# Optimization experiments

Hardware: AMD Instinct MI355X
Metric: run time of the kernel (lower is better)

Reference implementation:

```python
import jax, jax.numpy as jnp
import numpy as np

NEG_SLOPE = 0.2
K_L = 0.5
K_G = 0.5
TEMP_G = 1e-3


def _leaky(v):
    return jnp.where(v >= 0, v, NEG_SLOPE * v)


def _topk_row_mask(scores, keep):
    # scores: [n, n, h]; torch.topk(dim=0) -> indices [keep, n] per head,
    # then head_mask[indices, :] = 1 selects whole ROWS (any column hit).
    n = scores.shape[0]
    s = jnp.transpose(scores, (1, 2, 0))        # [n_cols, h, n_rows]
    _, idx = jax.lax.top_k(s, keep)             # [n_cols, h, keep]

    def per_head(idx_h):                        # idx_h: [n_cols, keep]
        return jnp.zeros((n,), scores.dtype).at[idx_h.reshape(-1)].set(1.0)

    rows = jax.vmap(per_head, in_axes=1, out_axes=0)(idx)  # [h, n_rows]
    return jnp.transpose(rows)[:, None, :]      # [n_rows, 1, h] broadcast over cols


def setup_inputs() -> dict:
    key = jax.random.key(0)
    ks = jax.random.split(key, 8)
    n, in_f, feat_dim = 1024, 256, 128
    H, F = 4, 64                                # n_heads, n_hidden (out_features=256)
    feats = jax.random.normal(ks[0], (n, feat_dim), dtype=jnp.float32)
    x = jax.random.normal(ks[1], (n, in_f), dtype=jnp.float32)
    adj = jax.random.randint(ks[2], (n, n, 1), 0, 2).astype(jnp.int32)
    sc = 0.05
    W_l = jax.random.normal(ks[3], (in_f, H * F), dtype=jnp.float32) * sc
    W_r = jax.random.normal(ks[4], (in_f, H * F), dtype=jnp.float32) * sc
    attn_w = jax.random.normal(ks[5], (F,), dtype=jnp.float32) * sc
    W_delta = jax.random.normal(ks[6], (2 * F, F), dtype=jnp.float32) * sc
    b_delta = jnp.zeros((F,), dtype=jnp.float32)
    return {"feats": feats, "x": x, "adj": adj, "W_l": W_l, "W_r": W_r,
            "attn_w": attn_w, "W_delta": W_delta, "b_delta": b_delta}


def reference(feats, x, adj, W_l, W_r, attn_w, W_delta, b_delta):
    n = x.shape[0]
    F = attn_w.shape[0]
    H = W_l.shape[1] // F
    g_l = (x @ W_l).reshape(n, H, F)
    g_r = (x @ W_r).reshape(n, H, F)
    # g_sum[i, j] = g_l[j] + g_r[i]  (repeat vs repeat_interleave ordering)
    g_sum = g_r[:, None, :, :] + g_l[None, :, :, :]          # [n, n, H, F]
    e = jnp.einsum('ijhf,f->ijh', _leaky(g_sum), attn_w)     # [n, n, H]

    mask_adj = adj > 0                                        # [n, n, 1]
    a_l = jax.nn.softmax(jnp.where(mask_adj, e, -jnp.inf), axis=1)
    a_1nd = a_l * mask_adj.astype(e.dtype)

    keep_l = int(n * (1.0 - K_L))
    a_filt = a_1nd * _topk_row_mask(a_1nd, keep_l)
    attn_local = jnp.einsum('ijh,jhf->ihf', a_filt, g_r)     # [n, H, F]

    omega = jax.nn.softmax(e, axis=1)
    fn = (feats - feats.min(axis=0)) / (feats.max(axis=0) - feats.min(axis=0))
    fn = jnp.where(jnp.isnan(fn), 0.0, fn)
    g_rn = (g_r - g_r.min(axis=0)) / (g_r.max(axis=0) - g_r.min(axis=0))
    nf = jnp.linalg.norm(fn, axis=1)                          # [n] (index j)
    ng = jnp.linalg.norm(g_rn, axis=2)                        # [n, H] (index i)
    alpha = jax.nn.softmax(jnp.abs(nf[None, :, None] - ng[:, None, :]), axis=1)
    gamma = 0.5 * (omega + (1.0 - alpha))

    keep_g = int(n * (1.0 - K_G))
    gf = gamma * _topk_row_mask(gamma, keep_g)
    gf = jax.nn.softmax(jnp.where(gf == 0, 1e-10, gf) / TEMP_G, axis=1)
    attn_global = jnp.einsum('ijh,jhf->ihf', gf, g_r)         # [n, H, F]

    inter = _leaky(jnp.concatenate([attn_local, attn_global], axis=2) @ W_delta + b_delta)
    delta = jax.nn.softmax(inter, axis=1)                     # softmax over heads (torch dim=1)
    attn_res = delta * attn_local + (1.0 - delta) * attn_global
    return attn_res.reshape(n, H * F)
```

## Files before the change

kernel.cpp:

```cpp
#include <hip/hip_runtime.h>
#include <cstdint>
#include <cstddef>

#define N 1024
#define HN 4
#define FDIM 64
#define KSEL 512
#define FLT_MAX_ 3.402823466e+38f

__device__ __forceinline__ float wred_sum(float v){
#pragma unroll
  for(int o=32;o>0;o>>=1) v += __shfl_down(v,o,64);
  return v;
}
__device__ __forceinline__ float bfly_sum(float v){
#pragma unroll
  for(int o=1;o<64;o<<=1) v += __shfl_xor(v,o,64);
  return v;
}
__device__ __forceinline__ float bfly_max(float v){
#pragma unroll
  for(int o=1;o<64;o<<=1) v = fmaxf(v,__shfl_xor(v,o,64));
  return v;
}
__device__ __forceinline__ int bfly_sumi(int v){
#pragma unroll
  for(int o=1;o<64;o<<=1) v += __shfl_xor(v,o,64);
  return v;
}
__device__ __forceinline__ float bred_sum(float v, float* scr){
  int t=threadIdx.x;
  v = wred_sum(v);
  __syncthreads();
  if((t&63)==0) scr[t>>6]=v;
  __syncthreads();
  return (scr[0]+scr[1])+(scr[2]+scr[3]);
}

__global__ __launch_bounds__(256) void stage1(const float* __restrict__ x,
                                              const float* __restrict__ W_l,
                                              const float* __restrict__ W_r,
                                              const int* __restrict__ adj,
                                              const float* __restrict__ feats,
                                              float* __restrict__ g_l,
                                              float* __restrict__ g_r,
                                              unsigned* __restrict__ adjbit,
                                              int* __restrict__ masks,
                                              float* __restrict__ pmin_f,
                                              float* __restrict__ pmax_f){
  int bx = blockIdx.x, t = threadIdx.x;
  if(bx < 512){
    const float* __restrict__ W = (bx >= 256) ? W_r : W_l;
    float* __restrict__ g = (bx >= 256) ? g_r : g_l;
    int i0 = (bx & 255)*4;
    float acc[4] = {0.f,0.f,0.f,0.f};
#pragma unroll 8
    for(int k=0;k<256;k++){
      float w = W[(size_t)k*256 + t];
#pragma unroll
      for(int r=0;r<4;r++) acc[r] = fmaf(x[(size_t)(i0+r)*256 + k], w, acc[r]);
    }
#pragma unroll
    for(int r=0;r<4;r++) g[(size_t)(i0+r)*256 + t] = acc[r];
  } else if(bx < 1536){
    int i = bx - 512, w = t>>6, lane = t&63;
    if(i < 32) masks[i*256 + t] = 0;
#pragma unroll
    for(int it=0; it<4; it++){
      int j = w*256 + it*64 + lane;
      int v = adj[(size_t)i*N + j];
      unsigned long long mb = __ballot(v > 0);
      if(lane == 0){
        adjbit[i*32 + w*8 + it*2]     = (unsigned)mb;
        adjbit[i*32 + w*8 + it*2 + 1] = (unsigned)(mb >> 32);
      }
    }
  } else {
    int chunk = bx - 1536;
    if(t < 128){
      float lo = FLT_MAX_, hi = -FLT_MAX_;
      int r0 = chunk*64;
      for(int r=0;r<64;r++){
        float v = feats[(size_t)(r0+r)*128 + t];
        lo = fminf(lo,v); hi = fmaxf(hi,v);
      }
      pmin_f[chunk*128+t]=lo; pmax_f[chunk*128+t]=hi;
    }
  }
}

__global__ __launch_bounds__(256) void stage2(const float* __restrict__ g_l,
                                              const float* __restrict__ g_r,
                                              const float* __restrict__ attn_w,
                                              const float* __restrict__ feats,
                                              const float* __restrict__ pmin_f, const float* __restrict__ pmax_f,
                                              float* __restrict__ pmin_g, float* __restrict__ pmax_g,
                                              float* __restrict__ nf,
                                              float* __restrict__ e){
  __shared__ __align__(16) float smem[2*64*68 + 128];
  int bx = blockIdx.x, t = threadIdx.x;
  if(bx < 1024){
    float* grs = smem;
    float* gls = smem + 64*68;
    float* aw  = smem + 2*64*68;
    float* aw2 = aw + 64;
    int h = bx >> 8, i0 = ((bx>>4)&15)*64, j0 = (bx&15)*64;
    if(t < 64){ float w = attn_w[t]; aw[t]=w; aw2[t]=0.2f*w; }
#pragma unroll
    for(int k=0;k<16;k++){
      int idx = t + k*256; int r = idx>>6, f = idx&63;
      grs[r*68+f] = g_r[(size_t)(i0+r)*256 + h*64 + f];
      gls[r*68+f] = g_l[(size_t)(j0+r)*256 + h*64 + f];
    }
    __syncthreads();
    int tj = t&15, ti = t>>4;
    float acc[4][4];
#pragma unroll
    for(int a=0;a<4;a++)
#pragma unroll
      for(int b=0;b<4;b++) acc[a][b]=0.f;
    for(int fc=0; fc<64; fc+=4){
      float4 wv  = *(float4*)&aw[fc];
      float4 wv2 = *(float4*)&aw2[fc];
      float4 ga4[4], gb4[4];
#pragma unroll
      for(int a=0;a<4;a++) ga4[a] = *(float4*)&grs[(ti*4+a)*68+fc];
#pragma unroll
      for(int b=0;b<4;b++) gb4[b] = *(float4*)&gls[(tj+16*b)*68+fc];
#pragma unroll
      for(int a=0;a<4;a++)
#pragma unroll
        for(int b=0;b<4;b++){
          float s0 = ga4[a].x + gb4[b].x;
          float s1 = ga4[a].y + gb4[b].y;
          float s2 = ga4[a].z + gb4[b].z;
          float s3 = ga4[a].w + gb4[b].w;
          acc[a][b] = fmaf(s0, (s0>=0.f)?wv.x:wv2.x, acc[a][b]);
          acc[a][b] = fmaf(s1, (s1>=0.f)?wv.y:wv2.y, acc[a][b]);
          acc[a][b] = fmaf(s2, (s2>=0.f)?wv.z:wv2.z, acc[a][b]);
          acc[a][b] = fmaf(s3, (s3>=0.f)?wv.w:wv2.w, acc[a][b]);
        }
    }
#pragma unroll
    for(int a=0;a<4;a++)
#pragma unroll
      for(int b=0;b<4;b++){
        int i = i0 + ti*4 + a, j = j0 + tj + 16*b;
        e[((size_t)h*N + i)*N + j] = acc[a][b];
      }
  } else if(bx < 1040){
    int chunk = bx - 1024;
    float lo = FLT_MAX_, hi = -FLT_MAX_;
    int r0 = chunk*64;
    for(int r=0;r<64;r++){
      float v = g_r[(size_t)(r0+r)*256 + t];
      lo = fminf(lo,v); hi = fmaxf(hi,v);
    }
    pmin_g[chunk*256+t]=lo; pmax_g[chunk*256+t]=hi;
  } else {
    int i = bx - 1040;
    float* scr = smem;
    float u = 0.f;
    if(t < 128){
      float lo = FLT_MAX_, hi = -FLT_MAX_;
#pragma unroll
      for(int k=0;k<16;k++){
        lo = fminf(lo, pmin_f[k*128+t]);
        hi = fmaxf(hi, pmax_f[k*128+t]);
      }
      float d = hi - lo;
      float v = feats[(size_t)i*128 + t];
      u = (d==0.f) ? 0.f : (v - lo)/d;
    }
    float tot = bred_sum(u*u, scr);
    if(t==0) nf[i] = sqrtf(tot);
  }
}

__global__ __launch_bounds__(256) void row_stats(const float* __restrict__ e,
                                                 const unsigned* __restrict__ adjbit,
                                                 const float* __restrict__ nf,
                                                 const float* __restrict__ g_r,
                                                 const float* __restrict__ pmin_g, const float* __restrict__ pmax_g,
                                                 float* __restrict__ ng,
                                                 float* __restrict__ mlA, float* __restrict__ islA,
                                                 float* __restrict__ moA, float* __restrict__ isoA,
                                                 float* __restrict__ maA, float* __restrict__ isaA,
                                                 float* __restrict__ mgA, float* __restrict__ sgA){
  int i = blockIdx.x, t = threadIdx.x, h = t>>6, lane = t&63;
  float glo = FLT_MAX_, ghi = -FLT_MAX_;
#pragma unroll
  for(int k=0;k<16;k++){
    glo = fminf(glo, pmin_g[k*256 + h*64 + lane]);
    ghi = fmaxf(ghi, pmax_g[k*256 + h*64 + lane]);
  }
  float dg = ghi - glo;
  float ug = (g_r[(size_t)i*256 + h*64 + lane] - glo)/dg;
  float ngv = sqrtf(bfly_sum(ug*ug));
  if(lane==0) ng[h*N + i] = ngv;

  size_t base = ((size_t)h*N + i)*N;
  float er[16], nfr[16];
  unsigned nib[4];
#pragma unroll
  for(int c=0;c<4;c++){
    float4 e4 = *(const float4*)(e  + base + c*256 + lane*4);
    float4 n4 = *(const float4*)(nf + c*256 + lane*4);
    er[c*4+0]=e4.x; er[c*4+1]=e4.y; er[c*4+2]=e4.z; er[c*4+3]=e4.w;
    nfr[c*4+0]=n4.x; nfr[c*4+1]=n4.y; nfr[c*4+2]=n4.z; nfr[c*4+3]=n4.w;
    nib[c] = (adjbit[i*32 + c*8 + (lane>>3)] >> ((lane&7)*4)) & 0xFu;
  }
  float ml=-FLT_MAX_, mo=-FLT_MAX_, ma=-FLT_MAX_;
#pragma unroll
  for(int c=0;c<4;c++)
#pragma unroll
    for(int k=0;k<4;k++){
      int q = c*4+k;
      float ev = er[q];
      mo = fmaxf(mo, ev);
      if((nib[c]>>k)&1) ml = fmaxf(ml, ev);
      ma = fmaxf(ma, fabsf(nfr[q]-ngv));
    }
  ml = bfly_max(ml); mo = bfly_max(mo); ma = bfly_max(ma);
  float sl=0.f, so=0.f, sa=0.f;
#pragma unroll
  for(int c=0;c<4;c++)
#pragma unroll
    for(int k=0;k<4;k++){
      int q = c*4+k;
      float ev = er[q];
      so += __expf(ev-mo);
      if((nib[c]>>k)&1) sl += __expf(ev-ml);
      sa += __expf(fabsf(nfr[q]-ngv)-ma);
    }
  sl = bfly_sum(sl); so = bfly_sum(so); sa = bfly_sum(sa);
  float isl = 1.f/sl, iso = 1.f/so, isa = 1.f/sa;
  float gg[16];
  float mg = -FLT_MAX_;
#pragma unroll
  for(int q=0;q<16;q++){
    float ev = er[q];
    float omega = __expf(ev-mo)*iso;
    float alpha = __expf(fabsf(nfr[q]-ngv)-ma)*isa;
    float g = 0.5f*(omega + 1.f - alpha);
    gg[q] = g;
    mg = fmaxf(mg, g);
  }
  mg = bfly_max(mg);
  float sg = 0.f;
#pragma unroll
  for(int q=0;q<16;q++) sg += __expf((gg[q]-mg)/1e-3f);
  sg = bfly_sum(sg);
  if(lane==0){
    mlA[h*N+i]=ml; islA[h*N+i]=isl;
    moA[h*N+i]=mo; isoA[h*N+i]=iso;
    maA[h*N+i]=ma; isaA[h*N+i]=isa;
    mgA[h*N+i]=mg; sgA[h*N+i]=sg;
  }
}

__global__ __launch_bounds__(256) void applyT(float* __restrict__ e,
                                              float* __restrict__ gamT,
                                              const unsigned* __restrict__ adjbit,
                                              const float* __restrict__ nf,
                                              const float* __restrict__ mlA, const float* __restrict__ islA,
                                              const float* __restrict__ moA, const float* __restrict__ isoA,
                                              const float* __restrict__ maA, const float* __restrict__ isaA,
                                              const float* __restrict__ ng){
  __shared__ __align__(16) float buf1[64][65];
  __shared__ __align__(16) float buf2[64][65];
  __shared__ __align__(16) float buf3[64][65];
  __shared__ float rml[64], risl[64], rmo[64], riso[64], rma[64], risa[64], rng[64], nfs[64];
  int h = blockIdx.y;
  int pp = blockIdx.x; int a = 0;
  while(pp >= 16 - a){ pp -= 16 - a; a++; }
  int b = a + pp;
  int t = threadIdx.x;
  int rg = t >> 4, c4 = t & 15;

  int i0 = a*64, j0 = b*64;
  if(t < 64){
    int o = h*N + i0 + t;
    rml[t]=mlA[o]; risl[t]=islA[o]; rmo[t]=moA[o]; riso[t]=isoA[o];
    rma[t]=maA[o]; risa[t]=isaA[o]; rng[t]=ng[o]; nfs[t]=nf[j0+t];
  }
  __syncthreads();
  float4 ev[4]; unsigned nb[4];
#pragma unroll
  for(int k=0;k<4;k++){
    int row = rg*4+k;
    ev[k] = *(const float4*)(e + ((size_t)h*N + i0+row)*N + j0 + c4*4);
    nb[k] = (adjbit[(size_t)(i0+row)*32 + (j0>>5) + (c4>>3)] >> ((c4&7)*4)) & 0xFu;
  }
#pragma unroll
  for(int k=0;k<4;k++){
    int row = rg*4+k;
    float ml=rml[row], isl=risl[row], mo=rmo[row], iso=riso[row];
    float ma=rma[row], isa=risa[row], ngv=rng[row];
    float evc[4] = {ev[k].x,ev[k].y,ev[k].z,ev[k].w};
#pragma unroll
    for(int c=0;c<4;c++){
      int j = c4*4+c;
      buf2[j][row] = ((nb[k]>>c)&1) ? __expf(evc[c]-ml)*isl : 0.f;
      float omega = __expf(evc[c]-mo)*iso;
      float alpha = __expf(fabsf(nfs[j]-ngv)-ma)*isa;
      buf1[j][row] = 0.5f*(omega + 1.f - alpha);
    }
  }
  __syncthreads();
#pragma unroll
  for(int k=0;k<4;k++){
    int jr = rg*4+k;
    *(float4*)(gamT + ((size_t)h*N + j0+jr)*N + i0 + c4*4) = *(float4*)&buf1[jr][c4*4];
  }
  if(a == b){
#pragma unroll
    for(int k=0;k<4;k++){
      int jr = rg*4+k;
      *(float4*)(e + ((size_t)h*N + j0+jr)*N + i0 + c4*4) = *(float4*)&buf2[jr][c4*4];
    }
    return;
  }
  int i1 = b*64, j1 = a*64;
  __syncthreads();
  if(t < 64){
    int o = h*N + i1 + t;
    rml[t]=mlA[o]; risl[t]=islA[o]; rmo[t]=moA[o]; riso[t]=isoA[o];
    rma[t]=maA[o]; risa[t]=isaA[o]; rng[t]=ng[o]; nfs[t]=nf[j1+t];
  }
#pragma unroll
  for(int k=0;k<4;k++){
    int row = rg*4+k;
    ev[k] = *(const float4*)(e + ((size_t)h*N + i1+row)*N + j1 + c4*4);
    nb[k] = (adjbit[(size_t)(i1+row)*32 + (j1>>5) + (c4>>3)] >> ((c4&7)*4)) & 0xFu;
  }
  __syncthreads();
#pragma unroll
  for(int k=0;k<4;k++){
    int jr = rg*4+k;
    *(float4*)(e + ((size_t)h*N + i1+jr)*N + j1 + c4*4) = *(float4*)&buf2[jr][c4*4];
  }
#pragma unroll
  for(int k=0;k<4;k++){
    int row = rg*4+k;
    float ml=rml[row], isl=risl[row], mo=rmo[row], iso=riso[row];
    float ma=rma[row], isa=risa[row], ngv=rng[row];
    float evc[4] = {ev[k].x,ev[k].y,ev[k].z,ev[k].w};
#pragma unroll
    for(int c=0;c<4;c++){
      int j = c4*4+c;
      buf3[j][row] = ((nb[k]>>c)&1) ? __expf(evc[c]-ml)*isl : 0.f;
      float omega = __expf(evc[c]-mo)*iso;
      float alpha = __expf(fabsf(nfs[j]-ngv)-ma)*isa;
      buf1[j][row] = 0.5f*(omega + 1.f - alpha);
    }
  }
  __syncthreads();
#pragma unroll
  for(int k=0;k<4;k++){
    int jr = rg*4+k;
    *(float4*)(gamT + ((size_t)h*N + j1+jr)*N + i1 + c4*4) = *(float4*)&buf1[jr][c4*4];
    *(float4*)(e    + ((size_t)h*N + j1+jr)*N + i1 + c4*4) = *(float4*)&buf3[jr][c4*4];
  }
}

__global__ __launch_bounds__(256) void colselect6(const float* __restrict__ a1T,
                                                  const float* __restrict__ gaT,
                                                  int* __restrict__ mask_l,
                                                  int* __restrict__ mask_g){
  __shared__ __align__(16) int hist[4][256];
  int t = threadIdx.x, w = t>>6, lane = t&63;
  int gcol = blockIdx.x*4 + w;
  int z  = gcol >> 12;
  int hj = gcol & 4095;
  int h  = hj >> 10;
  const float* __restrict__ src = (z ? gaT : a1T) + (size_t)hj * (size_t)N;
  int* __restrict__ mask = z ? mask_g : mask_l;
  int* hw = hist[w];

  unsigned ur[16];
#pragma unroll
  for(int c=0;c<4;c++){
    uint4 u4 = ((const uint4*)src)[c*64 + lane];
    ur[c*4+0]=u4.x; ur[c*4+1]=u4.y; ur[c*4+2]=u4.z; ur[c*4+3]=u4.w;
  }
  int np = 0;
#pragma unroll
  for(int q=0;q<16;q++) np += (ur[q] != 0u) ? 1 : 0;
  int cnt_pos = bfly_sumi(np);

  unsigned T; int tneed; int tiecnt = -1;
  if(cnt_pos < KSEL){
    T = 0u; tneed = KSEL - cnt_pos;
  } else {
    unsigned prefix = 0; int kth = KSEL;
#pragma unroll
    for(int b=3;b>=0;b--){
      *(int4*)&hw[lane*4] = make_int4(0,0,0,0);
#pragma unroll
      for(int q=0;q<16;q++){
        unsigned u = ur[q];
        bool act = (b==3) || ((u >> (8*(b+1))) == prefix);
        if(act){
          int bucket = (u >> (8*b)) & 0xFF;
          unsigned long long mball = __ballot(true);
          int lead = __ffsll(mball) - 1;
          int maj = __shfl(bucket, lead, 64);
          if(bucket == maj){
            int cnt = (int)__popcll(__ballot(true));
            if(lane == lead) atomicAdd(&hw[maj], cnt);
          } else {
            atomicAdd(&hw[bucket], 1);
          }
        }
      }
      int4 hv = *(int4*)&hw[lane*4];
      int s = hv.x+hv.y+hv.z+hv.w;
      int P = s;
#pragma unroll
      for(int off=1; off<64; off<<=1){
        int q2 = __shfl_up(P, off, 64);
        if(lane >= off) P += q2;
      }
      int total = __shfl(P, 63, 64);
      int suffChunk  = total - (P - s);
      int suffChunkN = total - P;
      bool cross = (suffChunk >= kth) && (suffChunkN < kth);
      int selb=0, newk=0, tcnt=0;
      if(cross){
        int s3 = suffChunkN + hv.w;
        int s2 = s3 + hv.z;
        int s1 = s2 + hv.y;
        if(s3 >= kth){ selb=4*lane+3; newk = kth - suffChunkN; tcnt=hv.w; }
        else if(s2 >= kth){ selb=4*lane+2; newk = kth - s3; tcnt=hv.z; }
        else if(s1 >= kth){ selb=4*lane+1; newk = kth - s2; tcnt=hv.y; }
        else { selb=4*lane; newk = kth - s1; tcnt=hv.x; }
      }
      unsigned long long cm = __ballot(cross);
      int csrc = __ffsll(cm) - 1;
      selb   = __shfl(selb, csrc, 64);
      kth    = __shfl(newk, csrc, 64);
      tiecnt = __shfl(tcnt, csrc, 64);
      prefix = (prefix << 8) | (unsigned)selb;
    }
    T = prefix; tneed = kth;
  }

  if(tiecnt == tneed){
#pragma unroll
    for(int c=0;c<4;c++)
#pragma unroll
      for(int k2=0;k2<4;k2++){
        int i = c*256 + lane*4 + k2;
        if(ur[c*4+k2] >= T) mask[h*N + i] = 1;
      }
  } else {
    int base = 0;
#pragma unroll
    for(int c=0;c<4;c++){
      int tc=0;
#pragma unroll
      for(int k2=0;k2<4;k2++) tc += (ur[c*4+k2]==T)?1:0;
      int pc = tc;
#pragma unroll
      for(int off=1; off<64; off<<=1){
        int q2 = __shfl_up(pc, off, 64);
        if(lane >= off) pc += q2;
      }
      int ctot = __shfl(pc, 63, 64);
      int run = base + pc - tc;
#pragma unroll
      for(int k2=0;k2<4;k2++){
        int i = c*256 + lane*4 + k2;
        unsigned u = ur[c*4+k2];
        bool sel = (u > T) || (u == T && run < tneed);
        run += (u==T)?1:0;
        if(sel) mask[h*N + i] = 1;
      }
      base += ctot;
    }
  }
}

__global__ __launch_bounds__(256) void attn_mm(const float* __restrict__ a1T,
                                               const float* __restrict__ gaT,
                                               const float* __restrict__ g_r,
                                               const float* __restrict__ mgA,
                                               const float* __restrict__ sgA,
                                               const int* __restrict__ mask_g,
                                               float* __restrict__ partL,
                                               float* __restrict__ partG){
  __shared__ __align__(16) float a_t[2][32][36];
  __shared__ __align__(16) float p_t[2][32][36];
  __shared__ __align__(16) float b_s[2][32][68];
  __shared__ float mgv[32], isgv[32];
  __shared__ int mgf[32];
  int i0 = blockIdx.x*32, h = blockIdx.y, s = blockIdx.z, j0 = s*128;
  int t = threadIdx.x;
  if(t < 32){
    mgv[t]  = mgA[h*N + i0 + t];
    isgv[t] = 1.f / sgA[h*N + i0 + t];
    mgf[t]  = mask_g[h*N + i0 + t];
  }
  int fq = t & 15, iq = t >> 4;
  int jj = t>>3, i4 = t&7, ii = i4*4;
  int jb2a = t>>4, d4a = t&15;
  int idxb = t + 256, jb2b = idxb>>4, d4b = idxb&15;

  float4 va, vg, vb0, vb1;
  {
    int jb = j0;
    size_t base = ((size_t)h*N + jb + jj)*N + i0 + i4*4;
    va  = *(const float4*)(a1T + base);
    vg  = *(const float4*)(gaT + base);
    vb0 = *(const float4*)(g_r + (size_t)(jb+jb2a)*256 + h*64 + d4a*4);
    vb1 = *(const float4*)(g_r + (size_t)(jb+jb2b)*256 + h*64 + d4b*4);
  }
  __syncthreads();
  {
    const float inv = 1.f/1024.f;
    *(float4*)&a_t[0][jj][i4*4] = va;
    float4 p4;
    p4.x = mgf[ii+0] ? __expf((vg.x - mgv[ii+0])/1e-3f)*isgv[ii+0] : inv;
    p4.y = mgf[ii+1] ? __expf((vg.y - mgv[ii+1])/1e-3f)*isgv[ii+1] : inv;
    p4.z = mgf[ii+2] ? __expf((vg.z - mgv[ii+2])/1e-3f)*isgv[ii+2] : inv;
    p4.w = mgf[ii+3] ? __expf((vg.w - mgv[ii+3])/1e-3f)*isgv[ii+3] : inv;
    *(float4*)&p_t[0][jj][i4*4] = p4;
    *(float4*)&b_s[0][jb2a][d4a*4] = vb0;
    *(float4*)&b_s[0][jb2b][d4b*4] = vb1;
  }
  float4 accL[2], accG[2];
#pragma unroll
  for(int r=0;r<2;r++){ accL[r]=make_float4(0,0,0,0); accG[r]=make_float4(0,0,0,0); }

  for(int sub=0; sub<4; sub++){
    int cur = sub & 1;
    __syncthreads();
    if(sub < 3){
      int jb = j0 + (sub+1)*32;
      size_t base = ((size_t)h*N + jb + jj)*N + i0 + i4*4;
      va  = *(const float4*)(a1T + base);
      vg  = *(const float4*)(gaT + base);
      vb0 = *(const float4*)(g_r + (size_t)(jb+jb2a)*256 + h*64 + d4a*4);
      vb1 = *(const float4*)(g_r + (size_t)(jb+jb2b)*256 + h*64 + d4b*4);
    }
#pragma unroll 8
    for(int j=0;j<32;j++){
      float4 bv = *(float4*)&b_s[cur][j][fq*4];
      float2 av = *(float2*)&a_t[cur][j][iq*2];
      float2 pv = *(float2*)&p_t[cur][j][iq*2];
      accL[0].x = fmaf(av.x, bv.x, accL[0].x); accL[0].y = fmaf(av.x, bv.y, accL[0].y);
      accL[0].z = fmaf(av.x, bv.z, accL[0].z); accL[0].w = fmaf(av.x, bv.w, accL[0].w);
      accL[1].x = fmaf(av.y, bv.x, accL[1].x); accL[1].y = fmaf(av.y, bv.y, accL[1].y);
      accL[1].z = fmaf(av.y, bv.z, accL[1].z); accL[1].w = fmaf(av.y, bv.w, accL[1].w);
      accG[0].x = fmaf(pv.x, bv.x, accG[0].x); accG[0].y = fmaf(pv.x, bv.y, accG[0].y);
      accG[0].z = fmaf(pv.x, bv.z, accG[0].z); accG[0].w = fmaf(pv.x, bv.w, accG[0].w);
      accG[1].x = fmaf(pv.y, bv.x, accG[1].x); accG[1].y = fmaf(pv.y, bv.y, accG[1].y);
      accG[1].z = fmaf(pv.y, bv.z, accG[1].z); accG[1].w = fmaf(pv.y, bv.w, accG[1].w);
    }
    if(sub < 3){
      int nxt = 1 - cur;
      const float inv = 1.f/1024.f;
      *(float4*)&a_t[nxt][jj][i4*4] = va;
      float4 p4;
      p4.x = mgf[ii+0] ? __expf((vg.x - mgv[ii+0])/1e-3f)*isgv[ii+0] : inv;
      p4.y = mgf[ii+1] ? __expf((vg.y - mgv[ii+1])/1e-3f)*isgv[ii+1] : inv;
      p4.z = mgf[ii+2] ? __expf((vg.z - mgv[ii+2])/1e-3f)*isgv[ii+2] : inv;
      p4.w = mgf[ii+3] ? __expf((vg.w - mgv[ii+3])/1e-3f)*isgv[ii+3] : inv;
      *(float4*)&p_t[nxt][jj][i4*4] = p4;
      *(float4*)&b_s[nxt][jb2a][d4a*4] = vb0;
      *(float4*)&b_s[nxt][jb2b][d4b*4] = vb1;
    }
  }
#pragma unroll
  for(int r=0;r<2;r++){
    int i = i0 + iq*2 + r;
    size_t o = ((size_t)s*N + i)*256 + h*64 + fq*4;
    *(float4*)&partL[o] = accL[r];
    *(float4*)&partG[o] = accG[r];
  }
}

__global__ __launch_bounds__(256) void epilogue(const float* __restrict__ partL,
                                                const float* __restrict__ partG,
                                                const int* __restrict__ mask_l,
                                                const float* __restrict__ W_delta,
                                                const float* __restrict__ b_delta,
                                                float* __restrict__ out){
  __shared__ float cat[4][128];
  __shared__ float inter_s[4][64];
  int i = blockIdx.x, t = threadIdx.x;
  int h = t>>6, f = t&63;
  float sl = 0.f, sg = 0.f;
#pragma unroll
  for(int s2=0;s2<8;s2++){
    size_t o = ((size_t)s2*N + i)*256 + h*64 + f;
    sl += partL[o];
    sg += partG[o];
  }
  if(!mask_l[h*N + i]) sl = 0.f;
  cat[h][f]      = sl;
  cat[h][64 + f] = sg;
  __syncthreads();
  float d = b_delta[f];
  for(int c=0;c<128;c++) d = fmaf(cat[h][c], W_delta[(size_t)c*64 + f], d);
  d = (d >= 0.f) ? d : 0.2f*d;
  inter_s[h][f] = d;
  __syncthreads();
  float m = inter_s[0][f];
#pragma unroll
  for(int hh=1;hh<4;hh++) m = fmaxf(m, inter_s[hh][f]);
  float ssum = 0.f;
#pragma unroll
  for(int hh=0;hh<4;hh++) ssum += __expf(inter_s[hh][f]-m);
  float delta = __expf(d - m)/ssum;
  out[(size_t)i*256 + h*64 + f] = delta*sl + (1.f - delta)*sg;
}

extern "C" void kernel_launch(void* const* d_in, const int* in_sizes, int n_in,
                              void* d_out, int out_size, void* d_ws, size_t ws_size,
                              hipStream_t stream) {
  const float* feats  = (const float*)d_in[0];
  const float* x      = (const float*)d_in[1];
  const int*   adj    = (const int*)  d_in[2];
  const float* W_l    = (const float*)d_in[3];
  const float* W_r    = (const float*)d_in[4];
  const float* attn_w = (const float*)d_in[5];
  const float* W_delta= (const float*)d_in[6];
  const float* b_delta= (const float*)d_in[7];
  float* out = (float*)d_out;

  float* ws = (float*)d_ws;
  size_t off = 0;
  float* g_l   = ws+off; off += (size_t)N*256;
  float* g_r   = ws+off; off += (size_t)N*256;
  float* e     = ws+off; off += (size_t)HN*N*N;
  float* gam   = ws+off; off += (size_t)HN*N*N;
  float* partL = ws+off; off += (size_t)8*N*256;
  float* partG = ws+off; off += (size_t)8*N*256;
  float* pmin_f= ws+off; off += 16*128;
  float* pmax_f= ws+off; off += 16*128;
  float* pmin_g= ws+off; off += 16*256;
  float* pmax_g= ws+off; off += 16*256;
  float* nf    = ws+off; off += N;
  float* ng    = ws+off; off += (size_t)HN*N;
  float* mlA   = ws+off; off += (size_t)HN*N;
  float* islA  = ws+off; off += (size_t)HN*N;
  float* moA   = ws+off; off += (size_t)HN*N;
  float* isoA  = ws+off; off += (size_t)HN*N;
  float* maA   = ws+off; off += (size_t)HN*N;
  float* isaA  = ws+off; off += (size_t)HN*N;
  float* mgA   = ws+off; off += (size_t)HN*N;
  float* sgA   = ws+off; off += (size_t)HN*N;
  int* mask_l  = (int*)(ws+off); off += (size_t)HN*N;
  int* mask_g  = (int*)(ws+off); off += (size_t)HN*N;
  unsigned* adjbit = (unsigned*)(ws+off); off += (size_t)N*32;

  stage1<<<1552, 256, 0, stream>>>(x, W_l, W_r, adj, feats, g_l, g_r, adjbit, mask_l, pmin_f, pmax_f);

  stage2<<<2064, 256, 0, stream>>>(g_l, g_r, attn_w, feats, pmin_f, pmax_f,
                                   pmin_g, pmax_g, nf, e);

  row_stats<<<N, 256, 0, stream>>>(e, adjbit, nf, g_r, pmin_g, pmax_g, ng,
                                   mlA, islA, moA, isoA, maA, isaA, mgA, sgA);

  applyT<<<dim3(136,HN), 256, 0, stream>>>(e, gam, adjbit, nf, mlA, islA, moA, isoA, maA, isaA, ng);

  colselect6<<<2048, 256, 0, stream>>>(e, gam, mask_l, mask_g);

  attn_mm<<<dim3(32,HN,8), 256, 0, stream>>>(e, gam, g_r, mgA, sgA, mask_g, partL, partG);

  epilogue<<<N, 256, 0, stream>>>(partL, partG, mask_l, W_delta, b_delta, out);
}
```

Before: 195.1 us.

## Write transposed logits in stage2 and recompute probabilities in select and matmul

Stage2 now also writes a transposed copy of the attention logits, staged through shared memory. This removes the applyT kernel, which materialised the transposed local-softmax and gamma matrices. The column top-k selection and the attention matmul now recompute the softmax, omega, alpha and gamma values directly from the transposed logits and the row statistics. That trades two 16 MB matrix writes and one extra launch for extra exp work, done twice, plus scalar strided loads of eT in the matmul.

New measurement: 199.9 us. 1.02x slower.

```diff
diff --git a/kernel.cpp b/kernel.cpp
--- a/kernel.cpp
+++ b/kernel.cpp
@@ -96,7 +96,8 @@
                                               const float* __restrict__ pmin_f, const float* __restrict__ pmax_f,
                                               float* __restrict__ pmin_g, float* __restrict__ pmax_g,
                                               float* __restrict__ nf,
-                                              float* __restrict__ e){
+                                              float* __restrict__ e,
+                                              float* __restrict__ eT){
   __shared__ __align__(16) float smem[2*64*68 + 128];
   int bx = blockIdx.x, t = threadIdx.x;
   if(bx < 1024){
@@ -148,6 +149,19 @@
         int i = i0 + ti*4 + a, j = j0 + tj + 16*b;
         e[((size_t)h*N + i)*N + j] = acc[a][b];
       }
+    __syncthreads();
+    float* esT = smem;
+#pragma unroll
+    for(int a=0;a<4;a++)
+#pragma unroll
+      for(int b=0;b<4;b++)
+        esT[(tj + 16*b)*68 + ti*4 + a] = acc[a][b];
+    __syncthreads();
+#pragma unroll
+    for(int k=0;k<4;k++){
+      int jl = (t>>4) + 16*k, ilx = (t&15)*4;
+      *(float4*)(eT + ((size_t)h*N + j0 + jl)*N + i0 + ilx) = *(float4*)&esT[jl*68 + ilx];
+    }
   } else if(bx < 1040){
     int chunk = bx - 1024;
     float lo = FLT_MAX_, hi = -FLT_MAX_;
@@ -259,131 +273,8 @@
   }
 }
 
-__global__ __launch_bounds__(256) void applyT(float* __restrict__ e,
-                                              float* __restrict__ gamT,
-                                              const unsigned* __restrict__ adjbit,
-                                              const float* __restrict__ nf,
-                                              const float* __restrict__ mlA, const float* __restrict__ islA,
-                                              const float* __restrict__ moA, const float* __restrict__ isoA,
-                                              const float* __restrict__ maA, const float* __restrict__ isaA,
-                                              const float* __restrict__ ng){
-  __shared__ __align__(16) float buf1[64][65];
-  __shared__ __align__(16) float buf2[64][65];
-  __shared__ __align__(16) float buf3[64][65];
-  __shared__ float rml[64], risl[64], rmo[64], riso[64], rma[64], risa[64], rng[64], nfs[64];
-  int h = blockIdx.y;
-  int pp = blockIdx.x; int a = 0;
-  while(pp >= 16 - a){ pp -= 16 - a; a++; }
-  int b = a + pp;
-  int t = threadIdx.x;
-  int rg = t >> 4, c4 = t & 15;
-
-  int i0 = a*64, j0 = b*64;
-  if(t < 64){
-    int o = h*N + i0 + t;
-    rml[t]=mlA[o]; risl[t]=islA[o]; rmo[t]=moA[o]; riso[t]=isoA[o];
-    rma[t]=maA[o]; risa[t]=isaA[o]; rng[t]=ng[o]; nfs[t]=nf[j0+t];
-  }
-  __syncthreads();
-  float4 ev[4]; unsigned nb[4];
-#pragma unroll
-  for(int k=0;k<4;k++){
-    int row = rg*4+k;
-    ev[k] = *(const float4*)(e + ((size_t)h*N + i0+row)*N + j0 + c4*4);
-    nb[k] = (adjbit[(size_t)(i0+row)*32 + (j0>>5) + (c4>>3)] >> ((c4&7)*4)) & 0xFu;
-  }
-#pragma unroll
-  for(int k=0;k<4;k++){
-    int row = rg*4+k;
-    float ml=rml[row], isl=risl[row], mo=rmo[row], iso=riso[row];
-    float ma=rma[row], isa=risa[row], ngv=rng[row];
-    float evc[4] = {ev[k].x,ev[k].y,ev[k].z,ev[k].w};
-#pragma unroll
-    for(int c=0;c<4;c++){
-      int j = c4*4+c;
-      buf2[j][row] = ((nb[k]>>c)&1) ? __expf(evc[c]-ml)*isl : 0.f;
-      float omega = __expf(evc[c]-mo)*iso;
-      float alpha = __expf(fabsf(nfs[j]-ngv)-ma)*isa;
-      buf1[j][row] = 0.5f*(omega + 1.f - alpha);
-    }
-  }
-  __syncthreads();
-#pragma unroll
-  for(int k=0;k<4;k++){
-    int jr = rg*4+k;
-    *(float4*)(gamT + ((size_t)h*N + j0+jr)*N + i0 + c4*4) = *(float4*)&buf1[jr][c4*4];
-  }
-  if(a == b){
-#pragma unroll
-    for(int k=0;k<4;k++){
-      int jr = rg*4+k;
-      *(float4*)(e + ((size_t)h*N + j0+jr)*N + i0 + c4*4) = *(float4*)&buf2[jr][c4*4];
-    }
-    return;
-  }
-  int i1 = b*64, j1 = a*64;
-  __syncthreads();
-  if(t < 64){
-    int o = h*N + i1 + t;
-    rml[t]=mlA[o]; risl[t]=islA[o]; rmo[t]=moA[o]; riso[t]=isoA[o];
-    rma[t]=maA[o]; risa[t]=isaA[o]; rng[t]=ng[o]; nfs[t]=nf[j1+t];
-  }
-#pragma unroll
-  for(int k=0;k<4;k++){
-    int row = rg*4+k;
-    ev[k] = *(const float4*)(e + ((size_t)h*N + i1+row)*N + j1 + c4*4);
-    nb[k] = (adjbit[(size_t)(i1+row)*32 + (j1>>5) + (c4>>3)] >> ((c4&7)*4)) & 0xFu;
-  }
-  __syncthreads();
-#pragma unroll
-  for(int k=0;k<4;k++){
-    int jr = rg*4+k;
-    *(float4*)(e + ((size_t)h*N + i1+jr)*N + j1 + c4*4) = *(float4*)&buf2[jr][c4*4];
-  }
-#pragma unroll
-  for(int k=0;k<4;k++){
-    int row = rg*4+k;
-    float ml=rml[row], isl=risl[row], mo=rmo[row], iso=riso[row];
-    float ma=rma[row], isa=risa[row], ngv=rng[row];
-    float evc[4] = {ev[k].x,ev[k].y,ev[k].z,ev[k].w};
-#pragma unroll
-    for(int c=0;c<4;c++){
-      int j = c4*4+c;
-      buf3[j][row] = ((nb[k]>>c)&1) ? __expf(evc[c]-ml)*isl : 0.f;
-      float omega = __expf(evc[c]-mo)*iso;
-      float alpha = __expf(fabsf(nfs[j]-ngv)-ma)*isa;
-      buf1[j][row] = 0.5f*(omega + 1.f - alpha);
-    }
-  }
-  __syncthreads();
-#pragma unroll
-  for(int k=0;k<4;k++){
-    int jr = rg*4+k;
-    *(float4*)(gamT + ((size_t)h*N + j1+jr)*N + i1 + c4*4) = *(float4*)&buf1[jr][c4*4];
-    *(float4*)(e    + ((size_t)h*N + j1+jr)*N + i1 + c4*4) = *(float4*)&buf3[jr][c4*4];
-  }
-}
-
-__global__ __launch_bounds__(256) void colselect6(const float* __restrict__ a1T,
-                                                  const float* __restrict__ gaT,
-                                                  int* __restrict__ mask_l,
-                                                  int* __restrict__ mask_g){
-  __shared__ __align__(16) int hist[4][256];
-  int t = threadIdx.x, w = t>>6, lane = t&63;
-  int gcol = blockIdx.x*4 + w;
-  int z  = gcol >> 12;
-  int hj = gcol & 4095;
-  int h  = hj >> 10;
-  const float* __restrict__ src = (z ? gaT : a1T) + (size_t)hj * (size_t)N;
-  int* __restrict__ mask = z ? mask_g : mask_l;
-  int* hw = hist[w];
-
-  unsigned ur[16];
-#pragma unroll
-  for(int c=0;c<4;c++){
-    uint4 u4 = ((const uint4*)src)[c*64 + lane];
-    ur[c*4+0]=u4.x; ur[c*4+1]=u4.y; ur[c*4+2]=u4.z; ur[c*4+3]=u4.w;
-  }
+__device__ __forceinline__ void select_top(const unsigned* ur, int* hw,
+                                           int* __restrict__ mask, int base, int lane){
   int np = 0;
 #pragma unroll
   for(int q=0;q<16;q++) np += (ur[q] != 0u) ? 1 : 0;
@@ -452,10 +343,10 @@
 #pragma unroll
       for(int k2=0;k2<4;k2++){
         int i = c*256 + lane*4 + k2;
-        if(ur[c*4+k2] >= T) mask[h*N + i] = 1;
+        if(ur[c*4+k2] >= T) mask[base + i] = 1;
       }
   } else {
-    int base = 0;
+    int run_base = 0;
 #pragma unroll
     for(int c=0;c<4;c++){
       int tc=0;
@@ -468,64 +359,140 @@
         if(lane >= off) pc += q2;
       }
       int ctot = __shfl(pc, 63, 64);
-      int run = base + pc - tc;
+      int run = run_base + pc - tc;
 #pragma unroll
       for(int k2=0;k2<4;k2++){
         int i = c*256 + lane*4 + k2;
         unsigned u = ur[c*4+k2];
         bool sel = (u > T) || (u == T && run < tneed);
         run += (u==T)?1:0;
-        if(sel) mask[h*N + i] = 1;
-      }
-      base += ctot;
-    }
-  }
-}
-
-__global__ __launch_bounds__(256) void attn_mm(const float* __restrict__ a1T,
-                                               const float* __restrict__ gaT,
-                                               const float* __restrict__ g_r,
-                                               const float* __restrict__ mgA,
-                                               const float* __restrict__ sgA,
-                                               const int* __restrict__ mask_g,
-                                               float* __restrict__ partL,
-                                               float* __restrict__ partG){
+        if(sel) mask[base + i] = 1;
+      }
+      run_base += ctot;
+    }
+  }
+}
+
+__global__ __launch_bounds__(256) void colselect7(const float* __restrict__ eT,
+                                                  const unsigned* __restrict__ adjbit,
+                                                  const float* __restrict__ nf,
+                                                  const float* __restrict__ mlA, const float* __restrict__ islA,
+                                                  const float* __restrict__ moA, const float* __restrict__ isoA,
+                                                  const float* __restrict__ maA, const float* __restrict__ isaA,
+                                                  const float* __restrict__ ngA,
+                                                  int* __restrict__ mask_l,
+                                                  int* __restrict__ mask_g){
+  __shared__ __align__(16) int hist[4][256];
+  int t = threadIdx.x, w = t>>6, lane = t&63;
+  int col = blockIdx.x*4 + w;
+  int h = col >> 10, jc = col & 1023;
+  const float* __restrict__ src = eT + (size_t)col * (size_t)N;
+
+  float ev[16];
+  unsigned abits = 0;
+  int wo = jc >> 5; unsigned bm = 1u << (jc & 31);
+#pragma unroll
+  for(int c=0;c<4;c++){
+    float4 e4 = ((const float4*)src)[c*64 + lane];
+    ev[c*4+0]=e4.x; ev[c*4+1]=e4.y; ev[c*4+2]=e4.z; ev[c*4+3]=e4.w;
+#pragma unroll
+    for(int k=0;k<4;k++){
+      int i = c*256 + lane*4 + k;
+      abits |= (adjbit[i*32 + wo] & bm) ? (1u << (c*4+k)) : 0u;
+    }
+  }
+  unsigned ur[16];
+#pragma unroll
+  for(int c=0;c<4;c++){
+    int ib = (h<<10) + c*256 + lane*4;
+    float4 ml4 = *(const float4*)(mlA+ib);
+    float4 il4 = *(const float4*)(islA+ib);
+    float mlv[4] = {ml4.x,ml4.y,ml4.z,ml4.w};
+    float ilv[4] = {il4.x,il4.y,il4.z,il4.w};
+#pragma unroll
+    for(int k=0;k<4;k++){
+      float a = ((abits>>(c*4+k))&1u) ? __expf(ev[c*4+k]-mlv[k])*ilv[k] : 0.f;
+      ur[c*4+k] = __float_as_uint(a);
+    }
+  }
+  select_top(ur, hist[w], mask_l, h<<10, lane);
+  float nfv = nf[jc];
+#pragma unroll
+  for(int c=0;c<4;c++){
+    int ib = (h<<10) + c*256 + lane*4;
+    float4 mo4 = *(const float4*)(moA+ib);
+    float4 io4 = *(const float4*)(isoA+ib);
+    float4 ma4 = *(const float4*)(maA+ib);
+    float4 ia4 = *(const float4*)(isaA+ib);
+    float4 ng4 = *(const float4*)(ngA+ib);
+    float mov[4]={mo4.x,mo4.y,mo4.z,mo4.w}, iov[4]={io4.x,io4.y,io4.z,io4.w};
+    float mav[4]={ma4.x,ma4.y,ma4.z,ma4.w}, iav[4]={ia4.x,ia4.y,ia4.z,ia4.w};
+    float ngv[4]={ng4.x,ng4.y,ng4.z,ng4.w};
+#pragma unroll
+    for(int k=0;k<4;k++){
+      float omega = __expf(ev[c*4+k]-mov[k])*iov[k];
+      float alpha = __expf(fabsf(nfv-ngv[k])-mav[k])*iav[k];
+      float g = 0.5f*(omega + 1.f - alpha);
+      ur[c*4+k] = __float_as_uint(g);
+    }
+  }
+  select_top(ur, hist[w], mask_g, h<<10, lane);
+}
+
+__global__ __launch_bounds__(256) void attn_mm2(const float* __restrict__ eT,
+                                                const float* __restrict__ g_r,
+                                                const unsigned* __restrict__ adjbit,
+                                                const float* __restrict__ nf,
+                                                const float* __restrict__ mlA, const float* __restrict__ islA,
+                                                const float* __restrict__ moA, const float* __restrict__ isoA,
+                                                const float* __restrict__ maA, const float* __restrict__ isaA,
+                                                const float* __restrict__ ngA,
+                                                const float* __restrict__ mgA, const float* __restrict__ sgA,
+                                                const int* __restrict__ mask_g,
+                                                float* __restrict__ partL,
+                                                float* __restrict__ partG){
   __shared__ __align__(16) float a_t[2][32][36];
   __shared__ __align__(16) float p_t[2][32][36];
   __shared__ __align__(16) float b_s[2][32][68];
-  __shared__ float mgv[32], isgv[32];
-  __shared__ int mgf[32];
   int i0 = blockIdx.x*32, h = blockIdx.y, s = blockIdx.z, j0 = s*128;
   int t = threadIdx.x;
-  if(t < 32){
-    mgv[t]  = mgA[h*N + i0 + t];
-    isgv[t] = 1.f / sgA[h*N + i0 + t];
-    mgf[t]  = mask_g[h*N + i0 + t];
-  }
+  int il = t & 31, jq = t >> 5;
+  int gi = h*N + i0 + il;
+  float ml_r = mlA[gi], il_r = islA[gi];
+  float mo_r = moA[gi], io_r = isoA[gi];
+  float ma_r = maA[gi], ia_r = isaA[gi];
+  float ng_r = ngA[gi];
+  float mg_r = mgA[gi], isg_r = 1.f/sgA[gi];
+  int   mgf_r = mask_g[gi];
   int fq = t & 15, iq = t >> 4;
-  int jj = t>>3, i4 = t&7, ii = i4*4;
   int jb2a = t>>4, d4a = t&15;
   int idxb = t + 256, jb2b = idxb>>4, d4b = idxb&15;
 
-  float4 va, vg, vb0, vb1;
+  float e0,e1,e2,e3; unsigned aw; float4 nf4, vb0, vb1;
   {
     int jb = j0;
-    size_t base = ((size_t)h*N + jb + jj)*N + i0 + i4*4;
-    va  = *(const float4*)(a1T + base);
-    vg  = *(const float4*)(gaT + base);
+    size_t ebase = ((size_t)h*N + jb + jq*4)*(size_t)N + i0 + il;
+    e0 = eT[ebase]; e1 = eT[ebase+N]; e2 = eT[ebase+2*N]; e3 = eT[ebase+3*N];
+    aw = adjbit[(size_t)(i0+il)*32 + s*4 + 0];
+    nf4 = *(const float4*)(nf + jb + jq*4);
     vb0 = *(const float4*)(g_r + (size_t)(jb+jb2a)*256 + h*64 + d4a*4);
     vb1 = *(const float4*)(g_r + (size_t)(jb+jb2b)*256 + h*64 + d4b*4);
   }
-  __syncthreads();
   {
     const float inv = 1.f/1024.f;
-    *(float4*)&a_t[0][jj][i4*4] = va;
-    float4 p4;
-    p4.x = mgf[ii+0] ? __expf((vg.x - mgv[ii+0])/1e-3f)*isgv[ii+0] : inv;
-    p4.y = mgf[ii+1] ? __expf((vg.y - mgv[ii+1])/1e-3f)*isgv[ii+1] : inv;
-    p4.z = mgf[ii+2] ? __expf((vg.z - mgv[ii+2])/1e-3f)*isgv[ii+2] : inv;
-    p4.w = mgf[ii+3] ? __expf((vg.w - mgv[ii+3])/1e-3f)*isgv[ii+3] : inv;
-    *(float4*)&p_t[0][jj][i4*4] = p4;
+    float evs[4] = {e0,e1,e2,e3};
+    float nfsv[4] = {nf4.x,nf4.y,nf4.z,nf4.w};
+#pragma unroll
+    for(int c=0;c<4;c++){
+      int jl = jq*4 + c;
+      float a = ((aw >> jl) & 1u) ? __expf(evs[c]-ml_r)*il_r : 0.f;
+      float omega = __expf(evs[c]-mo_r)*io_r;
+      float alpha = __expf(fabsf(nfsv[c]-ng_r)-ma_r)*ia_r;
+      float g = 0.5f*(omega + 1.f - alpha);
+      float p = mgf_r ? __expf((g-mg_r)/1e-3f)*isg_r : inv;
+      a_t[0][jl][il] = a;
+      p_t[0][jl][il] = p;
+    }
     *(float4*)&b_s[0][jb2a][d4a*4] = vb0;
     *(float4*)&b_s[0][jb2b][d4b*4] = vb1;
   }
@@ -538,9 +505,10 @@
     __syncthreads();
     if(sub < 3){
       int jb = j0 + (sub+1)*32;
-      size_t base = ((size_t)h*N + jb + jj)*N + i0 + i4*4;
-      va  = *(const float4*)(a1T + base);
-      vg  = *(const float4*)(gaT + base);
+      size_t ebase = ((size_t)h*N + jb + jq*4)*(size_t)N + i0 + il;
+      e0 = eT[ebase]; e1 = eT[ebase+N]; e2 = eT[ebase+2*N]; e3 = eT[ebase+3*N];
+      aw = adjbit[(size_t)(i0+il)*32 + s*4 + sub + 1];
+      nf4 = *(const float4*)(nf + jb + jq*4);
       vb0 = *(const float4*)(g_r + (size_t)(jb+jb2a)*256 + h*64 + d4a*4);
       vb1 = *(const float4*)(g_r + (size_t)(jb+jb2b)*256 + h*64 + d4b*4);
     }
@@ -561,13 +529,19 @@
     if(sub < 3){
       int nxt = 1 - cur;
       const float inv = 1.f/1024.f;
-      *(float4*)&a_t[nxt][jj][i4*4] = va;
-      float4 p4;
-      p4.x = mgf[ii+0] ? __expf((vg.x - mgv[ii+0])/1e-3f)*isgv[ii+0] : inv;
-      p4.y = mgf[ii+1] ? __expf((vg.y - mgv[ii+1])/1e-3f)*isgv[ii+1] : inv;
-      p4.z = mgf[ii+2] ? __expf((vg.z - mgv[ii+2])/1e-3f)*isgv[ii+2] : inv;
-      p4.w = mgf[ii+3] ? __expf((vg.w - mgv[ii+3])/1e-3f)*isgv[ii+3] : inv;
-      *(float4*)&p_t[nxt][jj][i4*4] = p4;
+      float evs[4] = {e0,e1,e2,e3};
+      float nfsv[4] = {nf4.x,nf4.y,nf4.z,nf4.w};
+#pragma unroll
+      for(int c=0;c<4;c++){
+        int jl = jq*4 + c;
+        float a = ((aw >> jl) & 1u) ? __expf(evs[c]-ml_r)*il_r : 0.f;
+        float omega = __expf(evs[c]-mo_r)*io_r;
+        float alpha = __expf(fabsf(nfsv[c]-ng_r)-ma_r)*ia_r;
+        float g = 0.5f*(omega + 1.f - alpha);
+        float p = mgf_r ? __expf((g-mg_r)/1e-3f)*isg_r : inv;
+        a_t[nxt][jl][il] = a;
+        p_t[nxt][jl][il] = p;
+      }
       *(float4*)&b_s[nxt][jb2a][d4a*4] = vb0;
       *(float4*)&b_s[nxt][jb2b][d4b*4] = vb1;
     }
@@ -635,7 +609,7 @@
   float* g_l   = ws+off; off += (size_t)N*256;
   float* g_r   = ws+off; off += (size_t)N*256;
   float* e     = ws+off; off += (size_t)HN*N*N;
-  float* gam   = ws+off; off += (size_t)HN*N*N;
+  float* eT    = ws+off; off += (size_t)HN*N*N;
   float* partL = ws+off; off += (size_t)8*N*256;
   float* partG = ws+off; off += (size_t)8*N*256;
   float* pmin_f= ws+off; off += 16*128;
@@ -659,16 +633,17 @@
   stage1<<<1552, 256, 0, stream>>>(x, W_l, W_r, adj, feats, g_l, g_r, adjbit, mask_l, pmin_f, pmax_f);
 
   stage2<<<2064, 256, 0, stream>>>(g_l, g_r, attn_w, feats, pmin_f, pmax_f,
-                                   pmin_g, pmax_g, nf, e);
+                                   pmin_g, pmax_g, nf, e, eT);
 
   row_stats<<<N, 256, 0, stream>>>(e, adjbit, nf, g_r, pmin_g, pmax_g, ng,
                                    mlA, islA, moA, isoA, maA, isaA, mgA, sgA);
 
-  applyT<<<dim3(136,HN), 256, 0, stream>>>(e, gam, adjbit, nf, mlA, islA, moA, isoA, maA, isaA, ng);
-
-  colselect6<<<2048, 256, 0, stream>>>(e, gam, mask_l, mask_g);
-
-  attn_mm<<<dim3(32,HN,8), 256, 0, stream>>>(e, gam, g_r, mgA, sgA, mask_g, partL, partG);
+  colselect7<<<1024, 256, 0, stream>>>(eT, adjbit, nf, mlA, islA, moA, isoA,
+                                       maA, isaA, ng, mask_l, mask_g);
+
+  attn_mm2<<<dim3(32,HN,8), 256, 0, stream>>>(eT, g_r, adjbit, nf,
+                                              mlA, islA, moA, isoA, maA, isaA, ng,
+                                              mgA, sgA, mask_g, partL, partG);
 
   epilogue<<<N, 256, 0, stream>>>(partL, partG, mask_l, W_delta, b_delta, out);
 }
```
